# Kernel optimization log

Measured on AMD Instinct MI355X. Metric: run time of the kernel, lower is better.

The kernel has to match this reference:

```python
import jax, jax.numpy as jnp
import numpy as np

# Mamba dims: d_model=1024, expand=2 -> d_inner=2048, d_state=16, d_conv=4, dt_rank=ceil(1024/16)=64
B, L, D = 2, 1024, 1024
DIN, N, R, K = 2048, 16, 64, 4
LN_EPS = 1e-5


def setup_inputs():
    key = jax.random.key(0)
    ks = jax.random.split(key, 12)
    s = lambda fan_in: 1.0 / np.sqrt(fan_in)
    inp = {
        "x": jax.random.normal(ks[0], (B, L, D), jnp.float32),
        "W_in": jax.random.normal(ks[1], (D, 2 * DIN), jnp.float32) * s(D),
        "conv_w": jax.random.normal(ks[2], (DIN, K), jnp.float32) * s(K),
        "conv_b": jax.random.normal(ks[3], (DIN,), jnp.float32) * 0.02,
        "W_x": jax.random.normal(ks[4], (DIN, R + 2 * N), jnp.float32) * s(DIN),
        "W_dt": jax.random.normal(ks[5], (R, DIN), jnp.float32) * s(R),
        # bias chosen so softplus(bias) ~ small positive dt
        "b_dt": jnp.full((DIN,), -4.0, jnp.float32)
        + jax.random.normal(ks[6], (DIN,), jnp.float32) * 0.1,
        # S4D-real init: A = -[1..N] broadcast over channels
        "A_log": jnp.log(jnp.broadcast_to(jnp.arange(1, N + 1, dtype=jnp.float32), (DIN, N))),
        "D_skip": jnp.ones((DIN,), jnp.float32),
        "W_out": jax.random.normal(ks[7], (DIN, D), jnp.float32) * s(DIN),
        "ln_g": jnp.ones((D,), jnp.float32),
        "ln_b": jnp.zeros((D,), jnp.float32),
    }
    return inp


def _silu(x):
    return x * jax.nn.sigmoid(x)


def _mamba_forward(x, W_in, conv_w, conv_b, W_x, W_dt, b_dt, A_log, D_skip, W_out, ln_g, ln_b):
    # in_proj -> (x_in, z), each [B, L, DIN]
    xz = jnp.einsum("bld,de->ble", x, W_in)
    x_in, z = jnp.split(xz, 2, axis=-1)

    # causal depthwise conv1d (kernel K=4) via shifted sums
    xp = jnp.pad(x_in, ((0, 0), (K - 1, 0), (0, 0)))  # [B, L+K-1, DIN]
    x_conv = conv_b
    for k in range(K):
        x_conv = x_conv + xp[:, k : k + L, :] * conv_w[:, k]
    x_conv = _silu(x_conv)  # [B, L, DIN]

    # x_proj -> dt_rank + 2*N
    x_dbl = jnp.einsum("bld,de->ble", x_conv, W_x)
    dt, Bc, Cc = jnp.split(x_dbl, [R, R + N], axis=-1)  # [B,L,R], [B,L,N], [B,L,N]
    delta = jax.nn.softplus(jnp.einsum("blr,rd->bld", dt, W_dt) + b_dt)  # [B,L,DIN]

    A = -jnp.exp(A_log)  # [DIN, N]
    # discretize: deltaA [B,L,DIN,N], deltaB_u [B,L,DIN,N]
    deltaA = jnp.exp(delta[..., None] * A)
    deltaBu = delta[..., None] * Bc[:, :, None, :] * x_conv[..., None]

    # selective scan over time
    def step(h, inp):
        dA, dBu, C_t = inp  # [B,DIN,N], [B,DIN,N], [B,N]
        h = dA * h + dBu
        y_t = jnp.einsum("bdn,bn->bd", h, C_t)
        return h, y_t

    h0 = jnp.zeros((B, DIN, N), jnp.float32)
    xs = (
        jnp.moveaxis(deltaA, 1, 0),
        jnp.moveaxis(deltaBu, 1, 0),
        jnp.moveaxis(Cc, 1, 0),
    )
    _, ys = jax.lax.scan(step, h0, xs)  # ys: [L, B, DIN]
    y = jnp.moveaxis(ys, 0, 1) + x_conv * D_skip  # [B, L, DIN]

    y = y * _silu(z)
    out = jnp.einsum("bld,de->ble", y, W_out)  # [B, L, D]

    # post LayerNorm
    mu = jnp.mean(out, axis=-1, keepdims=True)
    var = jnp.mean(jnp.square(out - mu), axis=-1, keepdims=True)
    return (out - mu) * jax.lax.rsqrt(var + LN_EPS) * ln_g + ln_b


def reference(x, W_in, conv_w, conv_b, W_x, W_dt, b_dt, A_log, D_skip, W_out, ln_g, ln_b):
    return _mamba_forward(x, W_in, conv_w, conv_b, W_x, W_dt, b_dt, A_log, D_skip, W_out, ln_g, ln_b)
```

## Files before the change

### kernel.cpp

```cpp
#include <hip/hip_runtime.h>

#define LSEQ 1024
#define DMODEL 1024
#define DINNER 2048
#define NSTATE 16
#define RRANK 64
#define CHUNK 32
#define NCHUNK 32
#define KSPLIT 8
#define MF (1024 * 1024)

typedef unsigned short u16;
typedef __attribute__((ext_vector_type(8))) short bf16x8;
typedef __attribute__((ext_vector_type(4))) short bf16x4;
typedef __attribute__((ext_vector_type(4))) float f32x4;

__device__ __forceinline__ float sigmoidf_(float x) {
    return 1.0f / (1.0f + __expf(-x));
}
__device__ __forceinline__ float softplusf_(float x) {
    return (x > 20.0f) ? x : log1pf(__expf(x));
}
__device__ __forceinline__ short f2bf(float f) {
    union { float f; unsigned u; } v; v.f = f;
    unsigned r = v.u + 0x7FFF + ((v.u >> 16) & 1);
    return (short)(r >> 16);
}
__device__ __forceinline__ float bf2f(u16 b) {
    union { unsigned u; float f; } v; v.u = ((unsigned)b) << 16;
    return v.f;
}
__device__ __forceinline__ void async_cp16(const u16* g, u16* l) {
    __builtin_amdgcn_global_load_lds(
        (const __attribute__((address_space(1))) unsigned int*)g,
        (__attribute__((address_space(3))) unsigned int*)l, 16, 0, 0);
}

__global__ __launch_bounds__(256) void cast_all_kernel(
    const float* __restrict__ x, u16* __restrict__ xb,
    const float* __restrict__ Win, u16* __restrict__ Wbin,
    const float* __restrict__ Wout, u16* __restrict__ Wbout)
{
    __shared__ float t[32][33];
    int bid = blockIdx.x;
    if (bid < 1024) {
        const size_t i = ((size_t)bid * 256 + threadIdx.x) * 8;
        float4 a = *(const float4*)&x[i];
        float4 b = *(const float4*)&x[i + 4];
        bf16x8 o;
        o[0] = f2bf(a.x); o[1] = f2bf(a.y); o[2] = f2bf(a.z); o[3] = f2bf(a.w);
        o[4] = f2bf(b.x); o[5] = f2bf(b.y); o[6] = f2bf(b.z); o[7] = f2bf(b.w);
        *(bf16x8*)&xb[i] = o;
        return;
    }
    const float* in; u16* out; int R, C, bxi, byi;
    if (bid < 1024 + 4096) {
        int tt = bid - 1024;
        in = Win; out = Wbin; R = DMODEL; C = 2 * DINNER;
        bxi = tt & 127; byi = tt >> 7;
    } else {
        int tt = bid - 5120;
        in = Wout; out = Wbout; R = DINNER; C = DMODEL;
        bxi = tt & 31; byi = tt >> 5;
    }
    const int bx = bxi * 32, by = byi * 32;
    const int tx = threadIdx.x & 31, ty = threadIdx.x >> 5;
    #pragma unroll
    for (int i = 0; i < 4; ++i)
        t[ty + 8 * i][tx] = in[(size_t)(by + ty + 8 * i) * C + bx + tx];
    __syncthreads();
    #pragma unroll
    for (int i = 0; i < 4; ++i)
        out[(size_t)(bx + ty + 8 * i) * R + by + tx] = (u16)f2bf(t[tx][ty + 8 * i]);
}

template<int BM, int BN, int BK, bool BF16OUT, int SWZ>
__global__ __launch_bounds__(256) void mfma_gemm_kernel(
    const u16* __restrict__ A, const u16* __restrict__ Bt,
    float* __restrict__ Cf, u16* __restrict__ Cb, int M, int N, int K)
{
    constexpr int WMS = BM / 32;
    constexpr int WNS = BN / 32;
    __shared__ u16 lA[BM * BK];
    __shared__ u16 lB[BN * BK];

    const int tid  = threadIdx.x;
    const int lane = tid & 63, wave = tid >> 6;
    const int quad = lane >> 4, l16 = lane & 15;
    const int wm   = (wave >> 1) * (BM / 2);
    const int wn   = (wave & 1) * (BN / 2);

    const int gx = gridDim.x, gy = gridDim.y;
    const int id = blockIdx.x + gx * blockIdx.y;
    const int G8 = (gx * gy) >> 3;
    const int id2 = (id & 7) * G8 + (id >> 3);
    int bx, by;
    if (SWZ == 1)      { bx = id2 / gy; by = id2 % gy; }
    else if (SWZ == 2) { by = id2 / gx; bx = id2 % gx; }
    else               { bx = blockIdx.x; by = blockIdx.y; }
    const int row0 = by * BM;
    const int col0 = bx * BN;

    f32x4 acc[WMS][WNS];
    #pragma unroll
    for (int i = 0; i < WMS; ++i)
        #pragma unroll
        for (int j = 0; j < WNS; ++j)
            acc[i][j] = (f32x4){0.f, 0.f, 0.f, 0.f};

    for (int k0 = 0; k0 < K; k0 += BK) {
        #pragma unroll
        for (int t = 0; t < (BM * BK) / 2048; ++t) {
            int c = tid + t * 256;
            int r = c / (BK / 8), kc = c % (BK / 8);
            async_cp16(&A[(size_t)(row0 + r) * K + k0 + kc * 8], &lA[c * 8]);
        }
        #pragma unroll
        for (int t = 0; t < (BN * BK) / 2048; ++t) {
            int c = tid + t * 256;
            int r = c / (BK / 8), kc = c % (BK / 8);
            async_cp16(&Bt[(size_t)(col0 + r) * K + k0 + kc * 8], &lB[c * 8]);
        }
        __syncthreads();
        #pragma unroll
        for (int ks = 0; ks < BK; ks += 32) {
            bf16x8 af[WMS], bfr[WNS];
            #pragma unroll
            for (int i = 0; i < WMS; ++i)
                af[i] = *(bf16x8*)&lA[(wm + i * 16 + l16) * BK + ks + quad * 8];
            #pragma unroll
            for (int j = 0; j < WNS; ++j)
                bfr[j] = *(bf16x8*)&lB[(wn + j * 16 + l16) * BK + ks + quad * 8];
            #pragma unroll
            for (int i = 0; i < WMS; ++i)
                #pragma unroll
                for (int j = 0; j < WNS; ++j)
                    acc[i][j] = __builtin_amdgcn_mfma_f32_16x16x32_bf16(
                        af[i], bfr[j], acc[i][j], 0, 0, 0);
        }
        __syncthreads();
    }
    if (BF16OUT) {
        #pragma unroll
        for (int i = 0; i < WMS; ++i)
            #pragma unroll
            for (int j = 0; j < WNS; ++j)
                #pragma unroll
                for (int r = 0; r < 4; ++r)
                    Cb[(size_t)(row0 + wm + i * 16 + quad * 4 + r) * N
                       + col0 + wn + j * 16 + l16] = (u16)f2bf(acc[i][j][r]);
    } else {
        #pragma unroll
        for (int i = 0; i < WMS; ++i)
            #pragma unroll
            for (int j = 0; j < WNS; ++j)
                #pragma unroll
                for (int r = 0; r < 4; ++r)
                    Cf[(size_t)(row0 + wm + i * 16 + quad * 4 + r) * N
                       + col0 + wn + j * 16 + l16] = acc[i][j][r];
    }
}

__global__ __launch_bounds__(256) void conv_silu_kernel(
    const u16* __restrict__ XZb, const float* __restrict__ cw,
    const float* __restrict__ cb, u16* __restrict__ xcb)
{
    const int idx = blockIdx.x * 256 + threadIdx.x;
    const int dq  = idx % (DINNER / 4);
    const int bl  = idx / (DINNER / 4);
    const int l   = bl % LSEQ;
    const int d0  = dq * 4;

    const float4* cw4 = (const float4*)cw;
    const float4 W0 = cw4[d0 + 0];
    const float4 W1 = cw4[d0 + 1];
    const float4 W2 = cw4[d0 + 2];
    const float4 W3 = cw4[d0 + 3];
    float4 s = *(const float4*)&cb[d0];

    #pragma unroll
    for (int k = 0; k < 4; ++k) {
        int ls = l + k - 3;
        if (ls >= 0) {
            bf16x4 xv = *(const bf16x4*)&XZb[(size_t)(bl + k - 3) * (2 * DINNER) + d0];
            s.x = fmaf(bf2f((u16)xv[0]), ((const float*)&W0)[k], s.x);
            s.y = fmaf(bf2f((u16)xv[1]), ((const float*)&W1)[k], s.y);
            s.z = fmaf(bf2f((u16)xv[2]), ((const float*)&W2)[k], s.z);
            s.w = fmaf(bf2f((u16)xv[3]), ((const float*)&W3)[k], s.w);
        }
    }
    bf16x4 o;
    o[0] = f2bf(s.x * sigmoidf_(s.x));
    o[1] = f2bf(s.y * sigmoidf_(s.y));
    o[2] = f2bf(s.z * sigmoidf_(s.z));
    o[3] = f2bf(s.w * sigmoidf_(s.w));
    *(bf16x4*)&xcb[(size_t)idx * 4] = o;
}

__global__ __launch_bounds__(256) void xproj_part_kernel(
    const u16* __restrict__ xcb, const float* __restrict__ Wx,
    float* __restrict__ part)
{
    __shared__ float As[32][64 + 4];
    __shared__ float Ws[32][96 + 4];

    const int tid  = threadIdx.x;
    const int tx   = tid % 32;
    const int ty   = tid / 32;
    const int row0 = blockIdx.x * 64;
    const int k0   = blockIdx.y * (DINNER / KSPLIT);

    float acc[8][3];
    #pragma unroll
    for (int i = 0; i < 8; ++i) { acc[i][0] = 0.f; acc[i][1] = 0.f; acc[i][2] = 0.f; }

    for (int kt = 0; kt < DINNER / KSPLIT; kt += 32) {
        const int kb = k0 + kt;
        {
            int m = tid >> 2, kq = tid & 3;
            bf16x8 v = *(const bf16x8*)&xcb[(size_t)(row0 + m) * DINNER + kb + kq * 8];
            #pragma unroll
            for (int j = 0; j < 8; ++j)
                As[kq * 8 + j][m] = bf2f((u16)v[j]);
        }
        #pragma unroll
        for (int i = 0; i < 3; ++i) {
            int lin = tid + i * 256;
            int kk = lin / 24, q = lin % 24;
            *(float4*)&Ws[kk][q * 4] = *(const float4*)&Wx[(size_t)(kb + kk) * 96 + q * 4];
        }
        __syncthreads();
        #pragma unroll 8
        for (int kk = 0; kk < 32; ++kk) {
            float a[8];
            *(float4*)&a[0] = *(const float4*)&As[kk][ty * 8];
            *(float4*)&a[4] = *(const float4*)&As[kk][ty * 8 + 4];
            float b0 = Ws[kk][tx], b1 = Ws[kk][tx + 32], b2 = Ws[kk][tx + 64];
            #pragma unroll
            for (int i = 0; i < 8; ++i) {
                acc[i][0] = fmaf(a[i], b0, acc[i][0]);
                acc[i][1] = fmaf(a[i], b1, acc[i][1]);
                acc[i][2] = fmaf(a[i], b2, acc[i][2]);
            }
        }
        __syncthreads();
    }
    float* po = part + (size_t)blockIdx.y * (2 * LSEQ * 96);
    #pragma unroll
    for (int i = 0; i < 8; ++i) {
        int r = row0 + ty * 8 + i;
        po[(size_t)r * 96 + tx]      = acc[i][0];
        po[(size_t)r * 96 + tx + 32] = acc[i][1];
        po[(size_t)r * 96 + tx + 64] = acc[i][2];
    }
}

__global__ __launch_bounds__(256) void delta_fused_kernel(
    const float* __restrict__ part, const float* __restrict__ Wdt,
    const float* __restrict__ bdt, u16* __restrict__ deltab,
    float* __restrict__ xBC)
{
    __shared__ float As[64][64 + 4];
    __shared__ float Ws[64][64 + 4];
    const int tid  = threadIdx.x;
    const int tx   = tid % 16;
    const int ty   = tid / 16;
    const int row0 = blockIdx.y * 64;
    const int col0 = blockIdx.x * 64;

    #pragma unroll
    for (int i = 0; i < 4; ++i) {
        int lin = tid + i * 256;
        int m = lin / 16, kq = lin % 16;
        float4 v = {0.f, 0.f, 0.f, 0.f};
        #pragma unroll
        for (int s8 = 0; s8 < KSPLIT; ++s8) {
            float4 p = *(const float4*)&part[(size_t)s8 * (2 * LSEQ * 96)
                                             + (size_t)(row0 + m) * 96 + kq * 4];
            v.x += p.x; v.y += p.y; v.z += p.z; v.w += p.w;
        }
        As[kq * 4 + 0][m] = v.x;
        As[kq * 4 + 1][m] = v.y;
        As[kq * 4 + 2][m] = v.z;
        As[kq * 4 + 3][m] = v.w;
    }
    #pragma unroll
    for (int i = 0; i < 4; ++i) {
        int lin = tid + i * 256;
        int kk = lin / 16, q = lin % 16;
        *(float4*)&Ws[kk][q * 4] = *(const float4*)&Wdt[(size_t)kk * DINNER + col0 + q * 4];
    }
    __syncthreads();

    float acc[4][4];
    #pragma unroll
    for (int i = 0; i < 4; ++i)
        #pragma unroll
        for (int j = 0; j < 4; ++j) acc[i][j] = 0.0f;

    #pragma unroll 8
    for (int kk = 0; kk < 64; ++kk) {
        float4 a = *(const float4*)&As[kk][ty * 4];
        float4 b = *(const float4*)&Ws[kk][tx * 4];
        const float* ap = (const float*)&a;
        const float* bp = (const float*)&b;
        #pragma unroll
        for (int i = 0; i < 4; ++i)
            #pragma unroll
            for (int j = 0; j < 4; ++j)
                acc[i][j] = fmaf(ap[i], bp[j], acc[i][j]);
    }

    float4 bv = *(const float4*)&bdt[col0 + tx * 4];
    const float* bvp = (const float*)&bv;
    #pragma unroll
    for (int i = 0; i < 4; ++i) {
        bf16x4 o;
        o[0] = f2bf(softplusf_(acc[i][0] + bvp[0]));
        o[1] = f2bf(softplusf_(acc[i][1] + bvp[1]));
        o[2] = f2bf(softplusf_(acc[i][2] + bvp[2]));
        o[3] = f2bf(softplusf_(acc[i][3] + bvp[3]));
        *(bf16x4*)&deltab[(size_t)(row0 + ty * 4 + i) * DINNER + col0 + tx * 4] = o;
    }

    if (blockIdx.x == 0) {
        #pragma unroll
        for (int i = 0; i < 8; ++i) {
            int lin = tid + i * 256;
            int r = lin >> 5, c2 = lin & 31;
            float s = 0.0f;
            #pragma unroll
            for (int s8 = 0; s8 < KSPLIT; ++s8)
                s += part[(size_t)s8 * (2 * LSEQ * 96)
                          + (size_t)(row0 + r) * 96 + RRANK + c2];
            xBC[(size_t)(row0 + r) * 32 + c2] = s;
        }
    }
}

__global__ __launch_bounds__(256) void scan_part1_kernel(
    const u16* __restrict__ deltab, const u16* __restrict__ xcb,
    const float* __restrict__ xBC, const float* __restrict__ A_log,
    float* __restrict__ Pbuf, float* __restrict__ Hbuf)
{
    const int d  = blockIdx.x * 256 + threadIdx.x;
    const int b  = blockIdx.y;
    const int ch = blockIdx.z;

    float Aa[NSTATE];
    #pragma unroll
    for (int q = 0; q < 4; ++q) {
        float4 v = *(const float4*)&A_log[(size_t)d * NSTATE + q * 4];
        Aa[q * 4 + 0] = -__expf(v.x);
        Aa[q * 4 + 1] = -__expf(v.y);
        Aa[q * 4 + 2] = -__expf(v.z);
        Aa[q * 4 + 3] = -__expf(v.w);
    }
    float h[NSTATE], P[NSTATE];
    #pragma unroll
    for (int n = 0; n < NSTATE; ++n) { h[n] = 0.0f; P[n] = 1.0f; }

    const size_t row0 = (size_t)b * LSEQ + (size_t)ch * CHUNK;
    #pragma unroll 4
    for (int t = 0; t < CHUNK; ++t) {
        const size_t row = row0 + t;
        float dv  = bf2f(deltab[row * DINNER + d]);
        float xcv = bf2f(xcb[row * DINNER + d]);
        float du  = dv * xcv;
        const float4* br = (const float4*)&xBC[row * 32];
        float4 B4[4] = { br[0], br[1], br[2], br[3] };
        const float* Bv = (const float*)B4;
        #pragma unroll
        for (int n = 0; n < NSTATE; ++n) {
            float dA = __expf(dv * Aa[n]);
            h[n] = fmaf(dA, h[n], du * Bv[n]);
            P[n] *= dA;
        }
    }
    float* Pp = &Pbuf[(((size_t)ch * 2 + b) * DINNER + d) * NSTATE];
    float* Hp = &Hbuf[(((size_t)ch * 2 + b) * DINNER + d) * NSTATE];
    #pragma unroll
    for (int q = 0; q < 4; ++q) {
        *(float4*)&Pp[q * 4] = *(float4*)&P[q * 4];
        *(float4*)&Hp[q * 4] = *(float4*)&h[q * 4];
    }
}

__global__ __launch_bounds__(256) void scan_combine_kernel(
    const float* __restrict__ Pbuf, const float* __restrict__ Hbuf,
    float* __restrict__ h0buf)
{
    const int idx = blockIdx.x * 256 + threadIdx.x;
    float H = 0.0f;
    #pragma unroll 8
    for (int cch = 0; cch < NCHUNK; ++cch) {
        const size_t g = (size_t)cch * (2 * DINNER * NSTATE) + idx;
        h0buf[g] = H;
        H = fmaf(Pbuf[g], H, Hbuf[g]);
    }
}

__global__ __launch_bounds__(256) void scan_part2_kernel(
    const u16* __restrict__ deltab, const u16* __restrict__ xcb,
    const float* __restrict__ xBC, const float* __restrict__ h0buf,
    const u16* __restrict__ XZb, u16* __restrict__ yb,
    const float* __restrict__ A_log, const float* __restrict__ Dskip)
{
    const int d  = blockIdx.x * 256 + threadIdx.x;
    const int b  = blockIdx.y;
    const int ch = blockIdx.z;

    float Aa[NSTATE];
    #pragma unroll
    for (int q = 0; q < 4; ++q) {
        float4 v = *(const float4*)&A_log[(size_t)d * NSTATE + q * 4];
        Aa[q * 4 + 0] = -__expf(v.x);
        Aa[q * 4 + 1] = -__expf(v.y);
        Aa[q * 4 + 2] = -__expf(v.z);
        Aa[q * 4 + 3] = -__expf(v.w);
    }
    const float Dd = Dskip[d];

    float h[NSTATE];
    const float* Hp = &h0buf[(((size_t)ch * 2 + b) * DINNER + d) * NSTATE];
    #pragma unroll
    for (int q = 0; q < 4; ++q)
        *(float4*)&h[q * 4] = *(const float4*)&Hp[q * 4];

    const size_t row0 = (size_t)b * LSEQ + (size_t)ch * CHUNK;
    #pragma unroll 2
    for (int t = 0; t < CHUNK; ++t) {
        const size_t row = row0 + t;
        float dv  = bf2f(deltab[row * DINNER + d]);
        float xcv = bf2f(xcb[row * DINNER + d]);
        float du  = dv * xcv;
        const float4* br = (const float4*)&xBC[row * 32];
        float4 BC[8] = { br[0], br[1], br[2], br[3], br[4], br[5], br[6], br[7] };
        const float* Bv = (const float*)BC;
        const float* Cv = Bv + NSTATE;
        float y = 0.0f;
        #pragma unroll
        for (int n = 0; n < NSTATE; ++n) {
            float dA = __expf(dv * Aa[n]);
            h[n] = fmaf(dA, h[n], du * Bv[n]);
            y = fmaf(h[n], Cv[n], y);
        }
        float zz = bf2f(XZb[row * (2 * DINNER) + DINNER + d]);
        float yv = (y + xcv * Dd) * (zz * sigmoidf_(zz));
        yb[row * DINNER + d] = (u16)f2bf(yv);
    }
}

__global__ __launch_bounds__(256) void ln_kernel(
    const float* __restrict__ t, const float* __restrict__ g,
    const float* __restrict__ b, float* __restrict__ out)
{
    const int row = blockIdx.x;
    const int tid = threadIdx.x;
    float4 v = *(const float4*)&t[(size_t)row * DMODEL + tid * 4];
    float s = v.x + v.y + v.z + v.w;
    float q = v.x * v.x + v.y * v.y + v.z * v.z + v.w * v.w;
    #pragma unroll
    for (int m = 1; m < 64; m <<= 1) {
        s += __shfl_xor(s, m, 64);
        q += __shfl_xor(q, m, 64);
    }
    __shared__ float ss[4], qq[4];
    if ((tid & 63) == 0) { ss[tid >> 6] = s; qq[tid >> 6] = q; }
    __syncthreads();
    float S = ss[0] + ss[1] + ss[2] + ss[3];
    float Q = qq[0] + qq[1] + qq[2] + qq[3];
    float mu  = S * (1.0f / DMODEL);
    float var = Q * (1.0f / DMODEL) - mu * mu;
    float rs  = rsqrtf(var + 1e-5f);
    float4 gv = *(const float4*)&g[tid * 4];
    float4 bv = *(const float4*)&b[tid * 4];
    float4 o;
    o.x = (v.x - mu) * rs * gv.x + bv.x;
    o.y = (v.y - mu) * rs * gv.y + bv.y;
    o.z = (v.z - mu) * rs * gv.z + bv.z;
    o.w = (v.w - mu) * rs * gv.w + bv.w;
    *(float4*)&out[(size_t)row * DMODEL + tid * 4] = o;
}

extern "C" void kernel_launch(void* const* d_in, const int* in_sizes, int n_in,
                              void* d_out, int out_size, void* d_ws, size_t ws_size,
                              hipStream_t stream) {
    const float* x      = (const float*)d_in[0];
    const float* W_in   = (const float*)d_in[1];
    const float* conv_w = (const float*)d_in[2];
    const float* conv_b = (const float*)d_in[3];
    const float* W_x    = (const float*)d_in[4];
    const float* W_dt   = (const float*)d_in[5];
    const float* b_dt   = (const float*)d_in[6];
    const float* A_log  = (const float*)d_in[7];
    const float* D_skip = (const float*)d_in[8];
    const float* W_out  = (const float*)d_in[9];
    const float* ln_g   = (const float*)d_in[10];
    const float* ln_b   = (const float*)d_in[11];
    (void)in_sizes; (void)n_in; (void)out_size; (void)ws_size;

    const int M = 2 * LSEQ;

    float* ws     = (float*)d_ws;
    u16*   XZb    = (u16*)ws;
    u16*   xcb    = (u16*)(ws + 4 * MF);
    u16*   deltab = (u16*)(ws + 6 * MF);
    float* part   = ws + 8 * (size_t)MF;
    float* Pbuf   = ws + 8 * (size_t)MF;
    float* Hbuf   = ws + 10 * (size_t)MF;
    float* h0     = ws + 12 * (size_t)MF;
    u16*   xb     = (u16*)(ws + 14 * MF);
    u16*   Wbin   = (u16*)(ws + 15 * MF);
    u16*   Wbout  = (u16*)(ws + 17 * MF);
    float* xBC    = ws + 18 * (size_t)MF;
    u16*   yb     = (u16*)(ws + 15 * MF);
    float* pout   = ws;

    cast_all_kernel<<<1024 + 4096 + 2048, 256, 0, stream>>>(
        x, xb, W_in, Wbin, W_out, Wbout);

    mfma_gemm_kernel<128, 128, 64, true, 1>
        <<<dim3((2 * DINNER) / 128, M / 128), 256, 0, stream>>>(
            xb, Wbin, nullptr, XZb, M, 2 * DINNER, DMODEL);

    conv_silu_kernel<<<(M * (DINNER / 4)) / 256, 256, 0, stream>>>(
        XZb, conv_w, conv_b, xcb);

    xproj_part_kernel<<<dim3(M / 64, KSPLIT), 256, 0, stream>>>(xcb, W_x, part);

    delta_fused_kernel<<<dim3(DINNER / 64, M / 64), 256, 0, stream>>>(
        part, W_dt, b_dt, deltab, xBC);

    scan_part1_kernel<<<dim3(DINNER / 256, 2, NCHUNK), 256, 0, stream>>>(
        deltab, xcb, xBC, A_log, Pbuf, Hbuf);
    scan_combine_kernel<<<(2 * DINNER * NSTATE) / 256, 256, 0, stream>>>(
        Pbuf, Hbuf, h0);
    scan_part2_kernel<<<dim3(DINNER / 256, 2, NCHUNK), 256, 0, stream>>>(
        deltab, xcb, xBC, h0, XZb, yb, A_log, D_skip);

    mfma_gemm_kernel<64, 64, 64, false, 2>
        <<<dim3(DMODEL / 64, M / 64), 256, 0, stream>>>(
            yb, Wbout, pout, nullptr, M, DMODEL, DINNER);

    ln_kernel<<<M, 256, 0, stream>>>(pout, ln_g, ln_b, (float*)d_out);
}
```

Baseline: 283.8 us.

## Move dt projection onto bf16 MFMA GEMM with fused softplus epilogue

The fp32 SIMT delta kernel is replaced by three pieces. A separate kernel reduces the x_proj split-K partials into a bf16 dt buffer plus xBC. W_dt is transposed and cast to bf16 in the cast kernel, and an MFMA GEMM with a bias+softplus epilogue writes delta. The block-index swizzle is also removed from the GEMM template, which changes L2 locality for the large GEMMs. The new path adds one launch and reduces dt precision to bf16.

Result: faster. 274.9 us (-3.1%).

```diff
diff --git a/kernel.cpp b/kernel.cpp
--- a/kernel.cpp
+++ b/kernel.cpp
@@ -39,7 +39,8 @@
 __global__ __launch_bounds__(256) void cast_all_kernel(
     const float* __restrict__ x, u16* __restrict__ xb,
     const float* __restrict__ Win, u16* __restrict__ Wbin,
-    const float* __restrict__ Wout, u16* __restrict__ Wbout)
+    const float* __restrict__ Wout, u16* __restrict__ Wbout,
+    const float* __restrict__ Wdt, u16* __restrict__ Wdtt)
 {
     __shared__ float t[32][33];
     int bid = blockIdx.x;
@@ -58,10 +59,14 @@
         int tt = bid - 1024;
         in = Win; out = Wbin; R = DMODEL; C = 2 * DINNER;
         bxi = tt & 127; byi = tt >> 7;
-    } else {
+    } else if (bid < 1024 + 4096 + 2048) {
         int tt = bid - 5120;
         in = Wout; out = Wbout; R = DINNER; C = DMODEL;
         bxi = tt & 31; byi = tt >> 5;
+    } else {
+        int tt = bid - 7168;
+        in = Wdt; out = Wdtt; R = RRANK; C = DINNER;
+        bxi = tt & 63; byi = tt >> 6;
     }
     const int bx = bxi * 32, by = byi * 32;
     const int tx = threadIdx.x & 31, ty = threadIdx.x >> 5;
@@ -74,10 +79,11 @@
         out[(size_t)(bx + ty + 8 * i) * R + by + tx] = (u16)f2bf(t[tx][ty + 8 * i]);
 }
 
-template<int BM, int BN, int BK, bool BF16OUT, int SWZ>
+template<int BM, int BN, int BK, int EPI>
 __global__ __launch_bounds__(256) void mfma_gemm_kernel(
     const u16* __restrict__ A, const u16* __restrict__ Bt,
-    float* __restrict__ Cf, u16* __restrict__ Cb, int M, int N, int K)
+    float* __restrict__ Cf, u16* __restrict__ Cb,
+    const float* __restrict__ bias, int M, int N, int K)
 {
     constexpr int WMS = BM / 32;
     constexpr int WNS = BN / 32;
@@ -89,17 +95,8 @@
     const int quad = lane >> 4, l16 = lane & 15;
     const int wm   = (wave >> 1) * (BM / 2);
     const int wn   = (wave & 1) * (BN / 2);
-
-    const int gx = gridDim.x, gy = gridDim.y;
-    const int id = blockIdx.x + gx * blockIdx.y;
-    const int G8 = (gx * gy) >> 3;
-    const int id2 = (id & 7) * G8 + (id >> 3);
-    int bx, by;
-    if (SWZ == 1)      { bx = id2 / gy; by = id2 % gy; }
-    else if (SWZ == 2) { by = id2 / gx; bx = id2 % gx; }
-    else               { bx = blockIdx.x; by = blockIdx.y; }
-    const int row0 = by * BM;
-    const int col0 = bx * BN;
+    const int row0 = blockIdx.y * BM;
+    const int col0 = blockIdx.x * BN;
 
     f32x4 acc[WMS][WNS];
     #pragma unroll
@@ -140,7 +137,16 @@
         }
         __syncthreads();
     }
-    if (BF16OUT) {
+    if (EPI == 0) {
+        #pragma unroll
+        for (int i = 0; i < WMS; ++i)
+            #pragma unroll
+            for (int j = 0; j < WNS; ++j)
+                #pragma unroll
+                for (int r = 0; r < 4; ++r)
+                    Cf[(size_t)(row0 + wm + i * 16 + quad * 4 + r) * N
+                       + col0 + wn + j * 16 + l16] = acc[i][j][r];
+    } else if (EPI == 1) {
         #pragma unroll
         for (int i = 0; i < WMS; ++i)
             #pragma unroll
@@ -151,13 +157,16 @@
                        + col0 + wn + j * 16 + l16] = (u16)f2bf(acc[i][j][r]);
     } else {
         #pragma unroll
-        for (int i = 0; i < WMS; ++i)
-            #pragma unroll
-            for (int j = 0; j < WNS; ++j)
+        for (int j = 0; j < WNS; ++j) {
+            float bj = bias[col0 + wn + j * 16 + l16];
+            #pragma unroll
+            for (int i = 0; i < WMS; ++i)
                 #pragma unroll
                 for (int r = 0; r < 4; ++r)
-                    Cf[(size_t)(row0 + wm + i * 16 + quad * 4 + r) * N
-                       + col0 + wn + j * 16 + l16] = acc[i][j][r];
+                    Cb[(size_t)(row0 + wm + i * 16 + quad * 4 + r) * N
+                       + col0 + wn + j * 16 + l16]
+                        = (u16)f2bf(softplusf_(acc[i][j][r] + bj));
+        }
     }
 }
 
@@ -255,87 +264,18 @@
     }
 }
 
-__global__ __launch_bounds__(256) void delta_fused_kernel(
-    const float* __restrict__ part, const float* __restrict__ Wdt,
-    const float* __restrict__ bdt, u16* __restrict__ deltab,
+__global__ __launch_bounds__(256) void xproj_reduce_kernel(
+    const float* __restrict__ part, u16* __restrict__ dtb,
     float* __restrict__ xBC)
 {
-    __shared__ float As[64][64 + 4];
-    __shared__ float Ws[64][64 + 4];
-    const int tid  = threadIdx.x;
-    const int tx   = tid % 16;
-    const int ty   = tid / 16;
-    const int row0 = blockIdx.y * 64;
-    const int col0 = blockIdx.x * 64;
-
-    #pragma unroll
-    for (int i = 0; i < 4; ++i) {
-        int lin = tid + i * 256;
-        int m = lin / 16, kq = lin % 16;
-        float4 v = {0.f, 0.f, 0.f, 0.f};
-        #pragma unroll
-        for (int s8 = 0; s8 < KSPLIT; ++s8) {
-            float4 p = *(const float4*)&part[(size_t)s8 * (2 * LSEQ * 96)
-                                             + (size_t)(row0 + m) * 96 + kq * 4];
-            v.x += p.x; v.y += p.y; v.z += p.z; v.w += p.w;
-        }
-        As[kq * 4 + 0][m] = v.x;
-        As[kq * 4 + 1][m] = v.y;
-        As[kq * 4 + 2][m] = v.z;
-        As[kq * 4 + 3][m] = v.w;
-    }
-    #pragma unroll
-    for (int i = 0; i < 4; ++i) {
-        int lin = tid + i * 256;
-        int kk = lin / 16, q = lin % 16;
-        *(float4*)&Ws[kk][q * 4] = *(const float4*)&Wdt[(size_t)kk * DINNER + col0 + q * 4];
-    }
-    __syncthreads();
-
-    float acc[4][4];
-    #pragma unroll
-    for (int i = 0; i < 4; ++i)
-        #pragma unroll
-        for (int j = 0; j < 4; ++j) acc[i][j] = 0.0f;
-
-    #pragma unroll 8
-    for (int kk = 0; kk < 64; ++kk) {
-        float4 a = *(const float4*)&As[kk][ty * 4];
-        float4 b = *(const float4*)&Ws[kk][tx * 4];
-        const float* ap = (const float*)&a;
-        const float* bp = (const float*)&b;
-        #pragma unroll
-        for (int i = 0; i < 4; ++i)
-            #pragma unroll
-            for (int j = 0; j < 4; ++j)
-                acc[i][j] = fmaf(ap[i], bp[j], acc[i][j]);
-    }
-
-    float4 bv = *(const float4*)&bdt[col0 + tx * 4];
-    const float* bvp = (const float*)&bv;
-    #pragma unroll
-    for (int i = 0; i < 4; ++i) {
-        bf16x4 o;
-        o[0] = f2bf(softplusf_(acc[i][0] + bvp[0]));
-        o[1] = f2bf(softplusf_(acc[i][1] + bvp[1]));
-        o[2] = f2bf(softplusf_(acc[i][2] + bvp[2]));
-        o[3] = f2bf(softplusf_(acc[i][3] + bvp[3]));
-        *(bf16x4*)&deltab[(size_t)(row0 + ty * 4 + i) * DINNER + col0 + tx * 4] = o;
-    }
-
-    if (blockIdx.x == 0) {
-        #pragma unroll
-        for (int i = 0; i < 8; ++i) {
-            int lin = tid + i * 256;
-            int r = lin >> 5, c2 = lin & 31;
-            float s = 0.0f;
-            #pragma unroll
-            for (int s8 = 0; s8 < KSPLIT; ++s8)
-                s += part[(size_t)s8 * (2 * LSEQ * 96)
-                          + (size_t)(row0 + r) * 96 + RRANK + c2];
-            xBC[(size_t)(row0 + r) * 32 + c2] = s;
-        }
-    }
+    const int idx = blockIdx.x * 256 + threadIdx.x;
+    const int r = idx / 96, c = idx % 96;
+    float s = 0.0f;
+    #pragma unroll
+    for (int k = 0; k < KSPLIT; ++k)
+        s += part[(size_t)k * (2 * LSEQ * 96) + idx];
+    if (c < RRANK) dtb[(size_t)r * RRANK + c] = (u16)f2bf(s);
+    else           xBC[(size_t)r * 32 + (c - RRANK)] = s;
 }
 
 __global__ __launch_bounds__(256) void scan_part1_kernel(
@@ -514,23 +454,27 @@
     u16*   Wbin   = (u16*)(ws + 15 * MF);
     u16*   Wbout  = (u16*)(ws + 17 * MF);
     float* xBC    = ws + 18 * (size_t)MF;
+    u16*   Wdtt   = (u16*)(ws + 18 * MF + 65536);
+    u16*   dtb    = (u16*)(ws + 18 * MF + 131072);
     u16*   yb     = (u16*)(ws + 15 * MF);
     float* pout   = ws;
 
-    cast_all_kernel<<<1024 + 4096 + 2048, 256, 0, stream>>>(
-        x, xb, W_in, Wbin, W_out, Wbout);
-
-    mfma_gemm_kernel<128, 128, 64, true, 1>
+    cast_all_kernel<<<1024 + 4096 + 2048 + 128, 256, 0, stream>>>(
+        x, xb, W_in, Wbin, W_out, Wbout, W_dt, Wdtt);
+
+    mfma_gemm_kernel<128, 128, 64, 1>
         <<<dim3((2 * DINNER) / 128, M / 128), 256, 0, stream>>>(
-            xb, Wbin, nullptr, XZb, M, 2 * DINNER, DMODEL);
+            xb, Wbin, nullptr, XZb, nullptr, M, 2 * DINNER, DMODEL);
 
     conv_silu_kernel<<<(M * (DINNER / 4)) / 256, 256, 0, stream>>>(
         XZb, conv_w, conv_b, xcb);
 
     xproj_part_kernel<<<dim3(M / 64, KSPLIT), 256, 0, stream>>>(xcb, W_x, part);
-
-    delta_fused_kernel<<<dim3(DINNER / 64, M / 64), 256, 0, stream>>>(
-        part, W_dt, b_dt, deltab, xBC);
+    xproj_reduce_kernel<<<(M * 96) / 256, 256, 0, stream>>>(part, dtb, xBC);
+
+    mfma_gemm_kernel<128, 128, 64, 2>
+        <<<dim3(DINNER / 128, M / 128), 256, 0, stream>>>(
+            dtb, Wdtt, nullptr, deltab, b_dt, M, DINNER, RRANK);
 
     scan_part1_kernel<<<dim3(DINNER / 256, 2, NCHUNK), 256, 0, stream>>>(
         deltab, xcb, xBC, A_log, Pbuf, Hbuf);
@@ -539,9 +483,9 @@
     scan_part2_kernel<<<dim3(DINNER / 256, 2, NCHUNK), 256, 0, stream>>>(
         deltab, xcb, xBC, h0, XZb, yb, A_log, D_skip);
 
-    mfma_gemm_kernel<64, 64, 64, false, 2>
+    mfma_gemm_kernel<64, 64, 64, 0>
         <<<dim3(DMODEL / 64, M / 64), 256, 0, stream>>>(
-            yb, Wbout, pout, nullptr, M, DMODEL, DINNER);
+            yb, Wbout, pout, nullptr, nullptr, M, DMODEL, DINNER);
 
     ln_kernel<<<M, 256, 0, stream>>>(pout, ln_g, ln_b, (float*)d_out);
 }
```
